# Kernel optimization log

Hardware: AMD Instinct MI355X
Metric: run time of the kernel (lower is better)

## Reference

```python
import jax, jax.numpy as jnp
import numpy as np

CH = 128
GROUPS = 8
EPS = 1e-5

def group_norm(x, w, b):
    B, C, H, W = x.shape
    g = x.reshape(B, GROUPS, C // GROUPS, H, W)
    mean = g.mean(axis=(2, 3, 4), keepdims=True)
    var = g.var(axis=(2, 3, 4), keepdims=True)
    g = (g - mean) * jax.lax.rsqrt(var + EPS)
    g = g.reshape(B, C, H, W)
    return g * w[None, :, None, None] + b[None, :, None, None]

def setup_inputs() -> dict:
    key = jax.random.key(0)
    ks = jax.random.split(key, 7)
    C = CH
    x = jax.random.normal(ks[0], (8, C, 64, 64), dtype=jnp.float32)
    gn_w = jnp.ones((C,), dtype=jnp.float32)
    gn_b = jnp.zeros((C,), dtype=jnp.float32)
    s = 1.0 / np.sqrt(C)
    qkv_w = jax.random.normal(ks[1], (3 * C, C), dtype=jnp.float32) * s
    qkv_b = jax.random.normal(ks[2], (3 * C,), dtype=jnp.float32) * 0.01
    proj_w = jax.random.normal(ks[3], (C, C), dtype=jnp.float32) * s
    proj_b = jax.random.normal(ks[4], (C,), dtype=jnp.float32) * 0.01
    return {"x": x, "gn_w": gn_w, "gn_b": gn_b, "qkv_w": qkv_w,
            "qkv_b": qkv_b, "proj_w": proj_w, "proj_b": proj_b}

def reference(x, gn_w, gn_b, qkv_w, qkv_b, proj_w, proj_b):
    B, C, H, W = x.shape
    h = group_norm(x, gn_w, gn_b)
    # 1x1 conv == per-pixel matmul over channels
    qkv = jnp.einsum('bchw,oc->bohw', h, qkv_w) + qkv_b[None, :, None, None]
    q, k, v = jnp.split(qkv.reshape(B, 3 * C, H * W), 3, axis=1)  # each [B,C,N]
    scale = C ** (-0.5)
    attn = jax.nn.softmax(jnp.einsum('bci,bcj->bij', q * scale, k), axis=-1)
    out = jnp.einsum('bij,bcj->bci', attn, v).reshape(B, C, H, W)
    out = jnp.einsum('bchw,oc->bohw', out, proj_w) + proj_b[None, :, None, None]
    return x + out
```

## Files before the change

### kernel.cpp

```cpp
#include <hip/hip_runtime.h>
#include <stdint.h>


typedef __attribute__((ext_vector_type(8))) short short8;
typedef __attribute__((ext_vector_type(4))) float f32x4;
typedef __attribute__((ext_vector_type(16))) float f32x16;

#define MFMA_BF16(a, b, c) __builtin_amdgcn_mfma_f32_16x16x32_bf16((a), (b), (c), 0, 0, 0)
#define MFMA32(a, b, c) __builtin_amdgcn_mfma_f32_32x32x16_bf16((a), (b), (c), 0, 0, 0)
#define EXP2(x) __builtin_amdgcn_exp2f(x)

#define QSCALE 0.12751743f

__device__ __forceinline__ unsigned short f2bf(float f) {
    unsigned int u = __builtin_bit_cast(unsigned int, f);
    u += 0x7FFFu + ((u >> 16) & 1u);
    return (unsigned short)(u >> 16);
}
__device__ __forceinline__ float bf2f(unsigned int lo16) {
    return __builtin_bit_cast(float, lo16 << 16);
}
__device__ __forceinline__ short8 ldg8(const unsigned short* p) {
    return __builtin_bit_cast(short8, *(const uint4*)p);
}

__global__ __launch_bounds__(256) void k_pre(const float* __restrict__ x,
                                             float* __restrict__ sums,
                                             const float* __restrict__ qkv_w,
                                             const float* __restrict__ proj_w,
                                             unsigned short* __restrict__ wq,
                                             unsigned short* __restrict__ wp) {
    if (blockIdx.x >= 1024) {
        int i = ((blockIdx.x - 1024) * 256 + threadIdx.x) * 4;
        const float* src; unsigned short* dst; int off;
        if (i < 49152) { src = qkv_w; dst = wq; off = i; }
        else           { src = proj_w; dst = wp; off = i - 49152; }
        float4 v = *(const float4*)(src + off);
        uint2 pk;
        pk.x = (unsigned int)f2bf(v.x) | ((unsigned int)f2bf(v.y) << 16);
        pk.y = (unsigned int)f2bf(v.z) | ((unsigned int)f2bf(v.w) << 16);
        *(uint2*)(dst + off) = pk;
        return;
    }
    int g     = blockIdx.x >> 4;
    int slice = blockIdx.x & 15;
    const float* p = x + (size_t)g * 65536 + slice * 4096;
    float s = 0.f, sq = 0.f;
#pragma unroll
    for (int i = 0; i < 4; ++i) {
        float4 v = *(const float4*)(p + threadIdx.x * 4 + i * 1024);
        s  += v.x + v.y + v.z + v.w;
        sq += v.x*v.x + v.y*v.y + v.z*v.z + v.w*v.w;
    }
#pragma unroll
    for (int m = 1; m < 64; m <<= 1) { s += __shfl_xor(s, m, 64); sq += __shfl_xor(sq, m, 64); }
    __shared__ float ss[4], ssq[4];
    int w = threadIdx.x >> 6;
    if ((threadIdx.x & 63) == 0) { ss[w] = s; ssq[w] = sq; }
    __syncthreads();
    if (threadIdx.x == 0) {
        atomicAdd(&sums[g * 2],     ss[0] + ss[1] + ss[2] + ss[3]);
        atomicAdd(&sums[g * 2 + 1], ssq[0] + ssq[1] + ssq[2] + ssq[3]);
    }
}

__global__ __launch_bounds__(256) void k_qkv(const float* __restrict__ x,
                                             const float* __restrict__ sums,
                                             const float* __restrict__ gn_w,
                                             const float* __restrict__ gn_b,
                                             const unsigned short* __restrict__ wq,
                                             const float* __restrict__ qkv_b,
                                             unsigned short* __restrict__ q_ws,
                                             unsigned short* __restrict__ k_ws,
                                             unsigned short* __restrict__ v_ws) {
    __shared__ unsigned short h_lds[64][136];
    const int tid  = threadIdx.x;
    const int b    = blockIdx.x >> 6;
    const int n0   = (blockIdx.x & 63) << 6;
    const int lane = tid & 63, wave = tid >> 6;
    const int l15  = lane & 15, q4 = lane >> 4;

    {
        int cb = tid >> 4;
        int nn = (tid & 15) << 2;
#pragma unroll
        for (int k = 0; k < 8; ++k) {
            int c = cb + (k << 4);
            float4 v = *(const float4*)(x + ((size_t)(b * 128 + c) << 12) + n0 + nn);
            int g = c >> 4;
            float ts = sums[(b * 8 + g) * 2];
            float tq = sums[(b * 8 + g) * 2 + 1];
            float mean = ts * (1.f / 65536.f);
            float var  = tq * (1.f / 65536.f) - mean * mean;
            float rstd = rsqrtf(var + 1e-5f);
            float ga = gn_w[c] * rstd;
            float be = gn_b[c] - mean * ga;
            h_lds[nn + 0][c] = f2bf(v.x * ga + be);
            h_lds[nn + 1][c] = f2bf(v.y * ga + be);
            h_lds[nn + 2][c] = f2bf(v.z * ga + be);
            h_lds[nn + 3][c] = f2bf(v.w * ga + be);
        }
    }
    __syncthreads();

    short8 bfrag[4][4];
#pragma unroll
    for (int nt = 0; nt < 4; ++nt)
#pragma unroll
        for (int ks = 0; ks < 4; ++ks)
            bfrag[nt][ks] = *(const short8*)&h_lds[nt * 16 + l15][ks * 32 + q4 * 8];

#pragma unroll
    for (int ot = 0; ot < 6; ++ot) {
        int o0 = wave * 96 + ot * 16;
        short8 af[4];
#pragma unroll
        for (int ks = 0; ks < 4; ++ks)
            af[ks] = ldg8(wq + (size_t)(o0 + l15) * 128 + ks * 32 + q4 * 8);

        if (o0 < 256) {
            float bias[4];
#pragma unroll
            for (int r = 0; r < 4; ++r) bias[r] = qkv_b[o0 + q4 * 4 + r];
            float qs = (o0 < 128) ? QSCALE : 1.0f;
#pragma unroll
            for (int nt = 0; nt < 4; ++nt) {
                f32x4 acc = {0.f, 0.f, 0.f, 0.f};
#pragma unroll
                for (int ks = 0; ks < 4; ++ks)
                    acc = MFMA_BF16(af[ks], bfrag[nt][ks], acc);
                int n = n0 + nt * 16 + l15;
                unsigned short* dst = (o0 < 128) ? q_ws : k_ws;
                int oo = (o0 < 128) ? o0 : (o0 - 128);
                unsigned int lo = (unsigned int)f2bf((acc[0] + bias[0]) * qs) |
                                  ((unsigned int)f2bf((acc[1] + bias[1]) * qs) << 16);
                unsigned int hi = (unsigned int)f2bf((acc[2] + bias[2]) * qs) |
                                  ((unsigned int)f2bf((acc[3] + bias[3]) * qs) << 16);
                uint2 pk; pk.x = lo; pk.y = hi;
                *(uint2*)&dst[((size_t)(b * 4096 + n) << 7) + oo + q4 * 4] = pk;
            }
        } else {
            int c = o0 - 256 + l15;
            float vb = qkv_b[o0 + l15];
            unsigned short* vrow = v_ws + ((size_t)(b * 128 + c) << 12) + n0;
#pragma unroll
            for (int nt = 0; nt < 4; ++nt) {
                f32x4 acc = {0.f, 0.f, 0.f, 0.f};
#pragma unroll
                for (int ks = 0; ks < 4; ++ks)
                    acc = MFMA_BF16(bfrag[nt][ks], af[ks], acc);
                unsigned int lo = (unsigned int)f2bf(acc[0] + vb) |
                                  ((unsigned int)f2bf(acc[1] + vb) << 16);
                unsigned int hi = (unsigned int)f2bf(acc[2] + vb) |
                                  ((unsigned int)f2bf(acc[3] + vb) << 16);
                uint2 pk; pk.x = lo; pk.y = hi;
                *(uint2*)&vrow[nt * 16 + q4 * 4] = pk;
            }
        }
    }
}

__global__ __launch_bounds__(256, 3) void k_attn_part(const unsigned short* __restrict__ q_ws,
                                                      const unsigned short* __restrict__ k_ws,
                                                      const unsigned short* __restrict__ v_ws,
                                                      unsigned short* __restrict__ o_part,
                                                      float* __restrict__ ml) {
    __shared__ unsigned short K_lds[64][136];
    __shared__ unsigned short V_lds[128][72];
    __shared__ unsigned short P_lds[64][72];
    __shared__ float Lp[128];

    const int tid   = threadIdx.x;
    const int chunk = blockIdx.x & 3;
    const int tile  = (blockIdx.x >> 2) & 63;
    const int b     = blockIdx.x >> 8;
    const int i0    = tile << 6;
    const int lane  = tid & 63, wave = tid >> 6;
    const int ih    = wave >> 1, jh = wave & 1;
    const int l31   = lane & 31, h = lane >> 5;

    short8 qf[8];
    {
        const unsigned short* qp =
            q_ws + ((size_t)(b * 4096 + i0 + ih * 32 + l31) << 7) + h * 8;
#pragma unroll
        for (int ks = 0; ks < 8; ++ks) qf[ks] = ldg8(qp + ks * 16);
    }

    f32x16 acc[2];
#pragma unroll
    for (int e = 0; e < 16; ++e) { acc[0][e] = 0.f; acc[1][e] = 0.f; }
    float l_run = 0.f;

    const unsigned short* kbase = k_ws + ((size_t)b << 19);
    const unsigned short* vsrc  = v_ws + ((size_t)b << 19) +
                                  ((size_t)(tid >> 1) << 12) + (tid & 1) * 32;

    for (int it = 0; it < 16; ++it) {
        int j0 = (chunk << 10) + (it << 6);
        __syncthreads();
        {
            const unsigned short* ksrc = kbase + ((size_t)j0 << 7);
#pragma unroll
            for (int i = 0; i < 4; ++i) {
                int f = i * 256 + tid;
                int row = f >> 4, q = (f & 15) << 3;
                *(uint4*)&K_lds[row][q] = *(const uint4*)(ksrc + f * 8);
            }
            const unsigned short* vp = vsrc + j0;
            uint4* vd = (uint4*)&V_lds[tid >> 1][(tid & 1) * 32];
#pragma unroll
            for (int k = 0; k < 4; ++k) vd[k] = *(const uint4*)(vp + k * 8);
        }
        __syncthreads();

        f32x16 s;
#pragma unroll
        for (int e = 0; e < 16; ++e) s[e] = 0.f;
#pragma unroll
        for (int ks = 0; ks < 8; ++ks) {
            short8 kf = *(const short8*)&K_lds[jh * 32 + l31][ks * 16 + h * 8];
            s = MFMA32(kf, qf[ks], s);
        }

        float pv[16];
#pragma unroll
        for (int e = 0; e < 16; ++e) pv[e] = EXP2(fminf(s[e], 30.f));
        l_run += (((pv[0] + pv[1]) + (pv[2] + pv[3])) +
                  ((pv[4] + pv[5]) + (pv[6] + pv[7]))) +
                 (((pv[8] + pv[9]) + (pv[10] + pv[11])) +
                  ((pv[12] + pv[13]) + (pv[14] + pv[15])));
        unsigned short* prow = &P_lds[ih * 32 + l31][jh * 32 + (h << 2)];
#pragma unroll
        for (int rr = 0; rr < 4; ++rr) {
            unsigned int lo = (unsigned int)f2bf(pv[rr * 4 + 0]) |
                              ((unsigned int)f2bf(pv[rr * 4 + 1]) << 16);
            unsigned int hi = (unsigned int)f2bf(pv[rr * 4 + 2]) |
                              ((unsigned int)f2bf(pv[rr * 4 + 3]) << 16);
            uint2 pk; pk.x = lo; pk.y = hi;
            *(uint2*)(prow + rr * 8) = pk;
        }
        __syncthreads();

#pragma unroll
        for (int ks = 0; ks < 4; ++ks) {
            short8 pf = *(const short8*)&P_lds[ih * 32 + l31][ks * 16 + h * 8];
#pragma unroll
            for (int ct = 0; ct < 2; ++ct) {
                short8 vf = *(const short8*)&V_lds[jh * 64 + ct * 32 + l31][ks * 16 + h * 8];
                acc[ct] = MFMA32(pf, vf, acc[ct]);
            }
        }
    }

    float l2 = l_run + __shfl_xor(l_run, 32);
    if (h == 0) Lp[jh * 64 + ih * 32 + l31] = l2;
    __syncthreads();

    size_t pbase = (size_t)((b * 64 + tile) * 4 + chunk) * 8192;
    float rl[16];
#pragma unroll
    for (int r = 0; r < 16; ++r) {
        int il = (r & 3) + ((r >> 2) << 3) + (h << 2);
        rl[r] = 1.0f / (Lp[ih * 32 + il] + Lp[64 + ih * 32 + il]);
    }
#pragma unroll
    for (int ct = 0; ct < 2; ++ct)
#pragma unroll
        for (int r = 0; r < 16; ++r) {
            int row = ih * 32 + (r & 3) + ((r >> 2) << 3) + (h << 2);
            o_part[pbase + (size_t)row * 128 + jh * 64 + ct * 32 + l31] =
                f2bf(acc[ct][r] * rl[r]);
        }
    if (tid < 64) {
        int mb = ((b * 64 + tile) * 4 + chunk) * 64;
        ml[mb + tid] = __log2f(Lp[tid] + Lp[64 + tid]);
    }
}

__global__ __launch_bounds__(256) void k_merge_proj(const unsigned short* __restrict__ o_part,
                                                    const float* __restrict__ ml,
                                                    const float* __restrict__ x,
                                                    const unsigned short* __restrict__ wp,
                                                    const float* __restrict__ proj_b,
                                                    float* __restrict__ out) {
    __shared__ unsigned short O_lds[64][136];
    __shared__ float wgt[64][4];
    const int tid  = threadIdx.x;
    const int b    = blockIdx.x >> 6;
    const int tile = blockIdx.x & 63;
    const int i0   = tile << 6;
    const int lane = tid & 63, wave = tid >> 6;
    const int l15  = lane & 15, q4 = lane >> 4;
    const int tb   = (b * 64 + tile) * 4;

    if (tid < 64) {
        float m0 = ml[(tb + 0) * 64 + tid], m1 = ml[(tb + 1) * 64 + tid];
        float m2 = ml[(tb + 2) * 64 + tid], m3 = ml[(tb + 3) * 64 + tid];
        float M = fmaxf(fmaxf(m0, m1), fmaxf(m2, m3));
        float w0 = EXP2(m0 - M), w1 = EXP2(m1 - M), w2 = EXP2(m2 - M), w3 = EXP2(m3 - M);
        float rW = 1.0f / (w0 + w1 + w2 + w3);
        wgt[tid][0] = w0 * rW; wgt[tid][1] = w1 * rW;
        wgt[tid][2] = w2 * rW; wgt[tid][3] = w3 * rW;
    }
    __syncthreads();

    {
        int n = tid >> 2, q = tid & 3;
        float w[4];
#pragma unroll
        for (int ch = 0; ch < 4; ++ch) w[ch] = wgt[n][ch];
#pragma unroll
        for (int g = 0; g < 4; ++g) {
            float acc[8];
#pragma unroll
            for (int e = 0; e < 8; ++e) acc[e] = 0.f;
#pragma unroll
            for (int ch = 0; ch < 4; ++ch) {
                const unsigned short* p =
                    o_part + (size_t)(tb + ch) * 8192 + (size_t)n * 128 + q * 32 + g * 8;
                uint4 v = *(const uint4*)p;
                float wc = w[ch];
                acc[0] += wc * bf2f(v.x & 0xFFFF); acc[1] += wc * bf2f(v.x >> 16);
                acc[2] += wc * bf2f(v.y & 0xFFFF); acc[3] += wc * bf2f(v.y >> 16);
                acc[4] += wc * bf2f(v.z & 0xFFFF); acc[5] += wc * bf2f(v.z >> 16);
                acc[6] += wc * bf2f(v.w & 0xFFFF); acc[7] += wc * bf2f(v.w >> 16);
            }
            uint4 pk;
            pk.x = (unsigned int)f2bf(acc[0]) | ((unsigned int)f2bf(acc[1]) << 16);
            pk.y = (unsigned int)f2bf(acc[2]) | ((unsigned int)f2bf(acc[3]) << 16);
            pk.z = (unsigned int)f2bf(acc[4]) | ((unsigned int)f2bf(acc[5]) << 16);
            pk.w = (unsigned int)f2bf(acc[6]) | ((unsigned int)f2bf(acc[7]) << 16);
            *(uint4*)&O_lds[n][q * 32 + g * 8] = pk;
        }
    }
    __syncthreads();

    short8 bfrag[4][4];
#pragma unroll
    for (int nt = 0; nt < 4; ++nt)
#pragma unroll
        for (int ks = 0; ks < 4; ++ks)
            bfrag[nt][ks] = *(const short8*)&O_lds[nt * 16 + l15][ks * 32 + q4 * 8];

#pragma unroll
    for (int ot = 0; ot < 2; ++ot) {
        int o0 = wave * 32 + ot * 16;
        short8 af[4];
#pragma unroll
        for (int ks = 0; ks < 4; ++ks)
            af[ks] = ldg8(wp + (size_t)(o0 + l15) * 128 + ks * 32 + q4 * 8);
        float pb[4];
#pragma unroll
        for (int r = 0; r < 4; ++r) pb[r] = proj_b[o0 + q4 * 4 + r];

#pragma unroll
        for (int nt = 0; nt < 4; ++nt) {
            f32x4 acc = {0.f, 0.f, 0.f, 0.f};
#pragma unroll
            for (int ks = 0; ks < 4; ++ks)
                acc = MFMA_BF16(af[ks], bfrag[nt][ks], acc);
#pragma unroll
            for (int r = 0; r < 4; ++r) {
                size_t idx = ((size_t)(b * 128 + o0 + q4 * 4 + r) << 12) + i0 + nt * 16 + l15;
                out[idx] = x[idx] + acc[r] + pb[r];
            }
        }
    }
}

extern "C" void kernel_launch(void* const* d_in, const int* in_sizes, int n_in,
                              void* d_out, int out_size, void* d_ws, size_t ws_size,
                              hipStream_t stream) {
    const float* x      = (const float*)d_in[0];
    const float* gn_w   = (const float*)d_in[1];
    const float* gn_b   = (const float*)d_in[2];
    const float* qkv_w  = (const float*)d_in[3];
    const float* qkv_b  = (const float*)d_in[4];
    const float* proj_w = (const float*)d_in[5];
    const float* proj_b = (const float*)d_in[6];
    float* out = (float*)d_out;

    char* ws = (char*)d_ws;
    float* sums           = (float*)ws;
    unsigned short* wq    = (unsigned short*)(ws + 4096);
    unsigned short* wp    = (unsigned short*)(ws + 4096 + 98304);
    unsigned short* q_ws  = (unsigned short*)(ws + ((size_t)1  << 20));
    unsigned short* k_ws  = (unsigned short*)(ws + ((size_t)9  << 20));
    unsigned short* v_ws  = (unsigned short*)(ws + ((size_t)17 << 20));
    unsigned short* o_part= (unsigned short*)(ws + ((size_t)25 << 20));
    float* ml             = (float*)(ws + ((size_t)57 << 20));

    hipMemsetAsync(sums, 0, 512, stream);
    k_pre<<<1088, 256, 0, stream>>>(x, sums, qkv_w, proj_w, wq, wp);
    k_qkv<<<512, 256, 0, stream>>>(x, sums, gn_w, gn_b, wq, qkv_b, q_ws, k_ws, v_ws);
    k_attn_part<<<2048, 256, 0, stream>>>(q_ws, k_ws, v_ws, o_part, ml);
    k_merge_proj<<<512, 256, 0, stream>>>(o_part, ml, x, wp, proj_b, out);
}
```

Before: 213.7 us.

## Prefetch next K/V tile into registers and use hardware bf16 pack conversion

The attention loop now loads the next iteration's K and V tiles from global memory into registers right after the current tile is written to LDS. This lets global load latency overlap with the QK and PV MFMA work instead of stalling at the top of each iteration. It also replaces the manual software bf16 rounding of P with the v_cvt_pk_bf16_f32 instruction. The cost is eight more uint4 registers per thread, which adds register pressure and may reduce occupancy.

```diff
diff --git a/kernel.cpp b/kernel.cpp
--- a/kernel.cpp
+++ b/kernel.cpp
@@ -22,6 +22,11 @@
 }
 __device__ __forceinline__ short8 ldg8(const unsigned short* p) {
     return __builtin_bit_cast(short8, *(const uint4*)p);
+}
+__device__ __forceinline__ unsigned int cvtpk(float lo, float hi) {
+    unsigned int r;
+    asm("v_cvt_pk_bf16_f32 %0, %1, %2" : "=v"(r) : "v"(lo), "v"(hi));
+    return r;
 }
 
 __global__ __launch_bounds__(256) void k_pre(const float* __restrict__ x,
@@ -196,23 +201,40 @@
     const unsigned short* vsrc  = v_ws + ((size_t)b << 19) +
                                   ((size_t)(tid >> 1) << 12) + (tid & 1) * 32;
 
+    uint4 kreg[4], vreg[4];
+    {
+        const unsigned short* ksrc = kbase + ((size_t)(chunk << 10) << 7);
+#pragma unroll
+        for (int i = 0; i < 4; ++i) kreg[i] = *(const uint4*)(ksrc + (i * 256 + tid) * 8);
+        const unsigned short* vp = vsrc + (chunk << 10);
+#pragma unroll
+        for (int k = 0; k < 4; ++k) vreg[k] = *(const uint4*)(vp + k * 8);
+    }
+
     for (int it = 0; it < 16; ++it) {
-        int j0 = (chunk << 10) + (it << 6);
         __syncthreads();
         {
-            const unsigned short* ksrc = kbase + ((size_t)j0 << 7);
 #pragma unroll
             for (int i = 0; i < 4; ++i) {
                 int f = i * 256 + tid;
                 int row = f >> 4, q = (f & 15) << 3;
-                *(uint4*)&K_lds[row][q] = *(const uint4*)(ksrc + f * 8);
-            }
-            const unsigned short* vp = vsrc + j0;
+                *(uint4*)&K_lds[row][q] = kreg[i];
+            }
             uint4* vd = (uint4*)&V_lds[tid >> 1][(tid & 1) * 32];
 #pragma unroll
-            for (int k = 0; k < 4; ++k) vd[k] = *(const uint4*)(vp + k * 8);
+            for (int k = 0; k < 4; ++k) vd[k] = vreg[k];
         }
         __syncthreads();
+
+        if (it < 15) {
+            int j1 = (chunk << 10) + ((it + 1) << 6);
+            const unsigned short* ksrc = kbase + ((size_t)j1 << 7);
+#pragma unroll
+            for (int i = 0; i < 4; ++i) kreg[i] = *(const uint4*)(ksrc + (i * 256 + tid) * 8);
+            const unsigned short* vp = vsrc + j1;
+#pragma unroll
+            for (int k = 0; k < 4; ++k) vreg[k] = *(const uint4*)(vp + k * 8);
+        }
 
         f32x16 s;
 #pragma unroll
@@ -233,11 +255,9 @@
         unsigned short* prow = &P_lds[ih * 32 + l31][jh * 32 + (h << 2)];
 #pragma unroll
         for (int rr = 0; rr < 4; ++rr) {
-            unsigned int lo = (unsigned int)f2bf(pv[rr * 4 + 0]) |
-                              ((unsigned int)f2bf(pv[rr * 4 + 1]) << 16);
-            unsigned int hi = (unsigned int)f2bf(pv[rr * 4 + 2]) |
-                              ((unsigned int)f2bf(pv[rr * 4 + 3]) << 16);
-            uint2 pk; pk.x = lo; pk.y = hi;
+            uint2 pk;
+            pk.x = cvtpk(pv[rr * 4 + 0], pv[rr * 4 + 1]);
+            pk.y = cvtpk(pv[rr * 4 + 2], pv[rr * 4 + 3]);
             *(uint2*)(prow + rr * 8) = pk;
         }
         __syncthreads();
```

After: 396.5 us. 1.86x slower.

## Double-buffer K/V tiles with direct global-to-LDS loads and XOR swizzle

Applied to the files above, without the earlier changes.

The attention-partial kernel now keeps two LDS buffers each for K and V and uses global_load_lds to prefetch the next tile while the current one is being computed. The padded LDS layout is replaced with an XOR swizzle to avoid bank conflicts, and float-to-bf16 packing uses the hardware v_cvt_pk_bf16_f32 instruction. The aim is to hide global load latency behind the MFMA work, at the cost of doubled LDS use and occupancy lowered from 3 to 2 blocks per CU in launch bounds. Visibility of the async LDS writes relies only on __syncthreads, with no explicit wait on outstanding loads.

```diff
diff --git a/kernel.cpp b/kernel.cpp
--- a/kernel.cpp
+++ b/kernel.cpp
@@ -22,6 +22,16 @@
 }
 __device__ __forceinline__ short8 ldg8(const unsigned short* p) {
     return __builtin_bit_cast(short8, *(const uint4*)p);
+}
+__device__ __forceinline__ unsigned int cvtpk(float lo, float hi) {
+    unsigned int r;
+    asm("v_cvt_pk_bf16_f32 %0, %1, %2" : "=v"(r) : "v"(lo), "v"(hi));
+    return r;
+}
+__device__ __forceinline__ void gload16(const void* g, void* l) {
+    __builtin_amdgcn_global_load_lds(
+        (__attribute__((address_space(1))) void*)g,
+        (__attribute__((address_space(3))) void*)l, 16, 0, 0);
 }
 
 __global__ __launch_bounds__(256) void k_pre(const float* __restrict__ x,
@@ -160,13 +170,15 @@
     }
 }
 
-__global__ __launch_bounds__(256, 3) void k_attn_part(const unsigned short* __restrict__ q_ws,
+__global__ __launch_bounds__(256, 2) void k_attn_part(const unsigned short* __restrict__ q_ws,
                                                       const unsigned short* __restrict__ k_ws,
                                                       const unsigned short* __restrict__ v_ws,
                                                       unsigned short* __restrict__ o_part,
                                                       float* __restrict__ ml) {
-    __shared__ unsigned short K_lds[64][136];
-    __shared__ unsigned short V_lds[128][72];
+    __shared__ unsigned short K0[64][128];
+    __shared__ unsigned short K1[64][128];
+    __shared__ unsigned short V0[128][64];
+    __shared__ unsigned short V1[128][64];
     __shared__ unsigned short P_lds[64][72];
     __shared__ float Lp[128];
 
@@ -192,66 +204,84 @@
     for (int e = 0; e < 16; ++e) { acc[0][e] = 0.f; acc[1][e] = 0.f; }
     float l_run = 0.f;
 
-    const unsigned short* kbase = k_ws + ((size_t)b << 19);
-    const unsigned short* vsrc  = v_ws + ((size_t)b << 19) +
-                                  ((size_t)(tid >> 1) << 12) + (tid & 1) * 32;
-
-    for (int it = 0; it < 16; ++it) {
-        int j0 = (chunk << 10) + (it << 6);
-        __syncthreads();
-        {
-            const unsigned short* ksrc = kbase + ((size_t)j0 << 7);
-#pragma unroll
-            for (int i = 0; i < 4; ++i) {
-                int f = i * 256 + tid;
-                int row = f >> 4, q = (f & 15) << 3;
-                *(uint4*)&K_lds[row][q] = *(const uint4*)(ksrc + f * 8);
-            }
-            const unsigned short* vp = vsrc + j0;
-            uint4* vd = (uint4*)&V_lds[tid >> 1][(tid & 1) * 32];
-#pragma unroll
-            for (int k = 0; k < 4; ++k) vd[k] = *(const uint4*)(vp + k * 8);
-        }
-        __syncthreads();
-
-        f32x16 s;
-#pragma unroll
-        for (int e = 0; e < 16; ++e) s[e] = 0.f;
-#pragma unroll
-        for (int ks = 0; ks < 8; ++ks) {
-            short8 kf = *(const short8*)&K_lds[jh * 32 + l31][ks * 16 + h * 8];
-            s = MFMA32(kf, qf[ks], s);
-        }
-
-        float pv[16];
-#pragma unroll
-        for (int e = 0; e < 16; ++e) pv[e] = EXP2(fminf(s[e], 30.f));
-        l_run += (((pv[0] + pv[1]) + (pv[2] + pv[3])) +
-                  ((pv[4] + pv[5]) + (pv[6] + pv[7]))) +
-                 (((pv[8] + pv[9]) + (pv[10] + pv[11])) +
-                  ((pv[12] + pv[13]) + (pv[14] + pv[15])));
-        unsigned short* prow = &P_lds[ih * 32 + l31][jh * 32 + (h << 2)];
-#pragma unroll
-        for (int rr = 0; rr < 4; ++rr) {
-            unsigned int lo = (unsigned int)f2bf(pv[rr * 4 + 0]) |
-                              ((unsigned int)f2bf(pv[rr * 4 + 1]) << 16);
-            unsigned int hi = (unsigned int)f2bf(pv[rr * 4 + 2]) |
-                              ((unsigned int)f2bf(pv[rr * 4 + 3]) << 16);
-            uint2 pk; pk.x = lo; pk.y = hi;
-            *(uint2*)(prow + rr * 8) = pk;
-        }
-        __syncthreads();
-
-#pragma unroll
-        for (int ks = 0; ks < 4; ++ks) {
-            short8 pf = *(const short8*)&P_lds[ih * 32 + l31][ks * 16 + h * 8];
-#pragma unroll
-            for (int ct = 0; ct < 2; ++ct) {
-                short8 vf = *(const short8*)&V_lds[jh * 64 + ct * 32 + l31][ks * 16 + h * 8];
-                acc[ct] = MFMA32(pf, vf, acc[ct]);
-            }
-        }
-    }
+    const unsigned short* kbase = k_ws + ((size_t)b << 19) + ((size_t)chunk << 17);
+    int ksrcChunk[4];
+#pragma unroll
+    for (int q = 0; q < 4; ++q) {
+        int c   = wave * 256 + q * 64 + lane;
+        int row = c >> 4;
+        ksrcChunk[q] = row * 16 + ((c & 15) ^ (row & 15));
+    }
+    const unsigned short* vbase = v_ws + ((size_t)b << 19) +
+        ((size_t)(wave * 32 + (lane >> 3)) << 12) +
+        ((((lane & 7) ^ (lane >> 3))) << 3) + (chunk << 10);
+
+#define STAGE(T, KD, VD)                                                              \
+  do {                                                                                \
+    _Pragma("unroll")                                                                 \
+    for (int q = 0; q < 4; ++q)                                                       \
+      gload16(kbase + (size_t)(T) * 8192 + ksrcChunk[q] * 8,                          \
+              (char*)(&KD[0][0]) + wave * 4096 + q * 1024);                           \
+    _Pragma("unroll")                                                                 \
+    for (int q = 0; q < 4; ++q)                                                       \
+      gload16(vbase + (size_t)q * 32768 + (T) * 64,                                   \
+              (char*)(&VD[0][0]) + (wave * 4 + q) * 1024);                            \
+  } while (0)
+
+    const int krow = jh * 32 + l31;
+    const int ksw  = krow & 15;
+    const int vsw  = l31 & 7;
+
+    STAGE(0, K0, V0);
+
+#define ATTN_ITER(IT, KR, VR, KP, VP)                                                 \
+  do {                                                                                \
+    __syncthreads(); \
+    if ((IT) < 15) STAGE((IT) + 1, KP, VP);      \
+    f32x16 s;           \
+    _Pragma("unroll")                                                                 \
+    for (int e = 0; e < 16; ++e) s[e] = 0.f;                                          \
+    _Pragma("unroll")                                                                 \
+    for (int ks = 0; ks < 8; ++ks) {                                                  \
+      short8 kf = *(const short8*)&KR[krow][((ks * 2 + h) ^ ksw) << 3];               \
+      s = MFMA32(kf, qf[ks], s);                                                      \
+    }                                                                                 \
+    float pv[16];                                        \
+    _Pragma("unroll")                                                                 \
+    for (int e = 0; e < 16; ++e) pv[e] = EXP2(fminf(s[e], 30.f));                     \
+    l_run += (((pv[0] + pv[1]) + (pv[2] + pv[3])) +                                   \
+              ((pv[4] + pv[5]) + (pv[6] + pv[7]))) +                                  \
+             (((pv[8] + pv[9]) + (pv[10] + pv[11])) +                                 \
+              ((pv[12] + pv[13]) + (pv[14] + pv[15])));                               \
+    {                                                                                 \
+      unsigned short* prow = &P_lds[ih * 32 + l31][jh * 32 + (h << 2)];               \
+      _Pragma("unroll")                                                               \
+      for (int rr = 0; rr < 4; ++rr) {                                                \
+        uint2 pk;                                                                     \
+        pk.x = cvtpk(pv[rr * 4 + 0], pv[rr * 4 + 1]);                                 \
+        pk.y = cvtpk(pv[rr * 4 + 2], pv[rr * 4 + 3]);                                 \
+        *(uint2*)(prow + rr * 8) = pk;                                                \
+      }                                                                               \
+    }                                                                                 \
+    __syncthreads();      \
+    _Pragma("unroll")                                                                 \
+    for (int ks = 0; ks < 4; ++ks) {                                                  \
+      short8 pf = *(const short8*)&P_lds[ih * 32 + l31][ks * 16 + h * 8];             \
+      _Pragma("unroll")                                                               \
+      for (int ct = 0; ct < 2; ++ct) {                                                \
+        short8 vf = *(const short8*)                                                  \
+            &VR[jh * 64 + ct * 32 + l31][((ks * 2 + h) ^ vsw) << 3];                  \
+        acc[ct] = MFMA32(pf, vf, acc[ct]);                                            \
+      }                                                                               \
+    }                                                                                 \
+  } while (0)
+
+    for (int ib = 0; ib < 8; ++ib) {
+        ATTN_ITER(ib * 2,     K0, V0, K1, V1);
+        ATTN_ITER(ib * 2 + 1, K1, V1, K0, V0);
+    }
+#undef ATTN_ITER
+#undef STAGE
 
     float l2 = l_run + __shfl_xor(l_run, 32);
     if (h == 0) Lp[jh * 64 + ih * 32 + l31] = l2;
```

After: 208.3 us. 2.5% less time.
